# Kernel optimization log

Hardware: AMD Instinct MI355X
Metric: run time of the kernel (lower is better)

## Reference

```python
import jax, jax.numpy as jnp
import numpy as np

N = 8192        # number of routed items
D_IN = 1024     # sub-op output feature size (identity sub-ops)
E = 1024        # encoding_size
K = 8           # number of ops / type keys


def setup_inputs() -> dict:
    key = jax.random.key(0)
    k1, k2, k3, k4 = jax.random.split(key, 4)
    x = jax.random.normal(k1, (N, D_IN), dtype=jnp.float32)
    type_ids = jax.random.randint(k2, (N,), 0, K, dtype=jnp.int64)
    # Stacked per-type Linear params: Ws[k] maps op-k features -> encoding.
    W = jax.random.normal(k3, (K, D_IN, E), dtype=jnp.float32) / np.sqrt(D_IN)
    b = jax.random.normal(k4, (K, E), dtype=jnp.float32) * 0.01
    return {"x": x, "type_ids": type_ids, "W": W, "b": b}


def reference(x, type_ids, W, b):
    # x: [N, D], type_ids: [N] in [0, K), W: [K, D, E], b: [K, E]
    k = W.shape[0]
    onehot = jax.nn.one_hot(type_ids, k, dtype=x.dtype)          # [N, K] routing mask
    y = jnp.einsum('nd,kde->kne', x, W) + b[:, None, :]          # [K, N, E] per-type Linear
    enc = jnp.einsum('kne,nk->ne', y, onehot)                    # scatter-combine by type
    # out[:, :E] = routed encoding; out[:, E+ki] = 1.0 for item's type (one-hot tail)
    return jnp.concatenate([enc, onehot], axis=-1)               # [N, E + K]
```

## Files before the change

kernel.cpp:

```cpp
#include <hip/hip_runtime.h>

#define N_ITEMS 8192
#define D_IN    1024
#define E_OUT   1024
#define K_TYPES 8
#define OUT_W   (E_OUT + K_TYPES)

#define XBF_OFF  34816
#define WBF_OFF  (XBF_OFF + 16777216)
#define WS_NEED  ((size_t)WBF_OFF + 16777216)

typedef __attribute__((ext_vector_type(8))) short          bf16x8;
typedef __attribute__((ext_vector_type(8))) unsigned short u16x8;
typedef __attribute__((ext_vector_type(4))) float          f32x4;

__device__ __forceinline__ unsigned short f2bf(float f) {
    unsigned int u = __float_as_uint(f);
    return (unsigned short)((u + 0x7FFFu + ((u >> 16) & 1u)) >> 16);
}

__device__ __forceinline__ void gload16(const void* g, void* l) {
    __builtin_amdgcn_global_load_lds(
        (const __attribute__((address_space(1))) unsigned int*)g,
        (__attribute__((address_space(3)))       unsigned int*)l, 16, 0, 0);
}


__global__ __launch_bounds__(256) void k_sortmeta(const int* __restrict__ tid,
                                                  int* __restrict__ ws) {
    __shared__ int cnt[K_TYPES];
    const int t = threadIdx.x;
    if (t < K_TYPES) { cnt[t] = 0; ws[8 + t] = 0; }
    __syncthreads();
    int c[K_TYPES];
    #pragma unroll
    for (int k = 0; k < K_TYPES; ++k) c[k] = 0;
    for (int it = 0; it < N_ITEMS / 256; ++it) {
        const int v = tid[it * 256 + t];
        #pragma unroll
        for (int k = 0; k < K_TYPES; ++k) c[k] += (v == k) ? 1 : 0;
    }
    #pragma unroll
    for (int k = 0; k < K_TYPES; ++k) atomicAdd(&cnt[k], c[k]);
    __syncthreads();
    if (t == 0) {
        int off = 0, nt = 0;
        for (int k = 0; k < K_TYPES; ++k) {
            ws[16 + k] = off;
            const int cc = cnt[k];
            for (int r = 0; r < cc; r += 128) {
                ws[32 + 2 * nt] = k;
                ws[33 + 2 * nt] = off + r;
                ++nt;
            }
            off += cc;
        }
        ws[24] = off;
        ws[25] = nt;
    }
}

__global__ __launch_bounds__(256) void k_convX(const float* __restrict__ X,
                                               const int*   __restrict__ tid,
                                               int* __restrict__ ws,
                                               float* __restrict__ out) {
    __shared__ int wcnt[4][K_TYPES];
    __shared__ int wbase[4][K_TYPES];
    const int t = threadIdx.x;
    const int b = blockIdx.x;
    unsigned short* Xbf = (unsigned short*)((char*)ws + XBF_OFF);

    const size_t c0 = (size_t)b * 8192 + (size_t)t * 8;
    float4 v[8];
    #pragma unroll
    for (int j = 0; j < 4; ++j) {
        v[2 * j]     = *(const float4*)(X + c0 + (size_t)j * 2048);
        v[2 * j + 1] = *(const float4*)(X + c0 + (size_t)j * 2048 + 4);
    }
    #pragma unroll
    for (int j = 0; j < 4; ++j) {
        u16x8 o;
        o[0] = f2bf(v[2 * j].x);     o[1] = f2bf(v[2 * j].y);
        o[2] = f2bf(v[2 * j].z);     o[3] = f2bf(v[2 * j].w);
        o[4] = f2bf(v[2 * j + 1].x); o[5] = f2bf(v[2 * j + 1].y);
        o[6] = f2bf(v[2 * j + 1].z); o[7] = f2bf(v[2 * j + 1].w);
        *(u16x8*)(Xbf + c0 + (size_t)j * 2048) = o;
    }
    if (b < 32) {
        const int n    = b * 256 + t;
        const int v2   = tid[n];
        const int lane = t & 63;
        const int wv   = t >> 6;
        int myrank = 0;
        int mycnt  = 0;
        #pragma unroll
        for (int k = 0; k < K_TYPES; ++k) {
            const unsigned long long mk = __ballot(v2 == k);
            if (v2 == k)
                myrank = (int)__popcll(mk & ((1ull << lane) - 1ull));
            if (lane == k)
                mycnt = (int)__popcll(mk);
        }
        if (lane < K_TYPES) wcnt[wv][lane] = mycnt;
        __syncthreads();
        if (t < K_TYPES) {
            const int tot = wcnt[0][t] + wcnt[1][t] + wcnt[2][t] + wcnt[3][t];
            int base = ws[16 + t] + atomicAdd(&ws[8 + t], tot);
            #pragma unroll
            for (int q = 0; q < 4; ++q) { wbase[q][t] = base; base += wcnt[q][t]; }
        }
        __syncthreads();
        ws[256 + wbase[wv][v2] + myrank] = n;

        float* o2 = out + (size_t)n * OUT_W + E_OUT;
        *(float4*)(o2)     = make_float4(v2 == 0 ? 1.f : 0.f, v2 == 1 ? 1.f : 0.f,
                                         v2 == 2 ? 1.f : 0.f, v2 == 3 ? 1.f : 0.f);
        *(float4*)(o2 + 4) = make_float4(v2 == 4 ? 1.f : 0.f, v2 == 5 ? 1.f : 0.f,
                                         v2 == 6 ? 1.f : 0.f, v2 == 7 ? 1.f : 0.f);
    }
}

__global__ __launch_bounds__(256) void k_convW(const float* __restrict__ W,
                                               int* __restrict__ ws) {
    __shared__ unsigned short T[64][72];
    const int t = threadIdx.x;
    const int b = blockIdx.x;
    unsigned short* Wbf = (unsigned short*)((char*)ws + WBF_OFF);

    const int tbase = b * 2;
    const int dl = t >> 2;
    const int eq = (t & 3) * 16;
    float4 va[2][4];
    int kk[2], dd0[2], ee0[2];
    #pragma unroll
    for (int s = 0; s < 2; ++s) {
        const int tt = tbase + s;
        kk[s]  = tt >> 8;
        const int rem = tt & 255;
        dd0[s] = (rem >> 4) << 6;
        ee0[s] = (rem & 15) << 6;
        const float* src = W + ((size_t)(kk[s] * 1024 + dd0[s] + dl)) * 1024 + ee0[s] + eq;
        #pragma unroll
        for (int q = 0; q < 4; ++q)
            va[s][q] = *(const float4*)(src + q * 4);
    }
    const int el = t >> 2;
    const int dq = (t & 3) * 16;
    #pragma unroll
    for (int s = 0; s < 2; ++s) {
        if (s) __syncthreads();
        #pragma unroll
        for (int q = 0; q < 4; ++q) {
            T[eq + q * 4 + 0][dl] = f2bf(va[s][q].x);
            T[eq + q * 4 + 1][dl] = f2bf(va[s][q].y);
            T[eq + q * 4 + 2][dl] = f2bf(va[s][q].z);
            T[eq + q * 4 + 3][dl] = f2bf(va[s][q].w);
        }
        __syncthreads();
        unsigned short* dst = Wbf + ((size_t)kk[s] << 20)
                            + (size_t)(ee0[s] + el) * 1024 + dd0[s] + dq;
        *(u16x8*)(dst)     = *(const u16x8*)&T[el][dq];
        *(u16x8*)(dst + 8) = *(const u16x8*)&T[el][dq + 8];
    }
}

__global__ __launch_bounds__(256) void k_gemm_bf16(const float* __restrict__ Bias,
                                                   const int* __restrict__ ws,
                                                   float* __restrict__ out) {
    __shared__ unsigned short As[128 * 64];
    __shared__ unsigned short Bs[64 * 64];

    const int tile = blockIdx.x;
    if (tile >= ws[25]) return;
    const int ktype     = ws[32 + 2 * tile];
    const int row_start = ws[33 + 2 * tile];
    const int rows      = min(128, ws[17 + ktype] - row_start);
    const int* __restrict__ sorted = ws + 256 + row_start;
    const int bn0 = blockIdx.y * 64;

    const unsigned short* __restrict__ Xbf =
        (const unsigned short*)((const char*)ws + XBF_OFF);
    const unsigned short* __restrict__ Wbf =
        (const unsigned short*)((const char*)ws + WBF_OFF);

    const int t    = threadIdx.x;
    const int lane = t & 63;
    const int w    = t >> 6;
    const int wr   = w >> 1, wc = w & 1;

    const int srow = lane >> 3;
    const int skq  = (lane & 7) * 8;

    const unsigned short* gA[4];
    unsigned short* lA[4];
    #pragma unroll
    for (int i = 0; i < 4; ++i) {
        const int ar = w * 32 + i * 8 + srow;
        const int cr = sorted[ar < rows ? ar : rows - 1];
        gA[i] = Xbf + (size_t)cr * 1024 + skq;
        lA[i] = As + (w * 32 + i * 8) * 64;
    }
    const unsigned short* gB[2];
    unsigned short* lB[2];
    #pragma unroll
    for (int i = 0; i < 2; ++i) {
        const int er = bn0 + w * 16 + i * 8 + srow;
        gB[i] = Wbf + ((size_t)ktype << 20) + (size_t)er * 1024 + skq;
        lB[i] = Bs + (w * 16 + i * 8) * 64;
    }

    const int frow = lane & 15;
    const int fko  = (lane >> 4) * 8;
    const unsigned short* aB  = As + (wr * 64 + frow) * 64 + fko;
    const unsigned short* bBp = Bs + (wc * 32 + frow) * 64 + fko;

    f32x4 acc[4][2];
    #pragma unroll
    for (int m = 0; m < 4; ++m)
        #pragma unroll
        for (int n = 0; n < 2; ++n)
            acc[m][n] = (f32x4){0.f, 0.f, 0.f, 0.f};

    for (int k0 = 0; k0 < D_IN; k0 += 64) {
        #pragma unroll
        for (int i = 0; i < 4; ++i) gload16(gA[i] + k0, lA[i]);
        #pragma unroll
        for (int i = 0; i < 2; ++i) gload16(gB[i] + k0, lB[i]);
        __syncthreads();
        bf16x8 af[2][4], bf_[2][2];
        #pragma unroll
        for (int ks = 0; ks < 2; ++ks) {
            #pragma unroll
            for (int m = 0; m < 4; ++m)
                af[ks][m]  = *(const bf16x8*)(aB  + m * 16 * 64 + ks * 32);
            #pragma unroll
            for (int n = 0; n < 2; ++n)
                bf_[ks][n] = *(const bf16x8*)(bBp + n * 16 * 64 + ks * 32);
        }
        #pragma unroll
        for (int ks = 0; ks < 2; ++ks)
            #pragma unroll
            for (int m = 0; m < 4; ++m)
                #pragma unroll
                for (int n = 0; n < 2; ++n)
                    acc[m][n] = __builtin_amdgcn_mfma_f32_16x16x32_bf16(
                        af[ks][m], bf_[ks][n], acc[m][n], 0, 0, 0);
        __syncthreads();
    }

    const int col = lane & 15;
    const int rq  = (lane >> 4) * 4;
    float bv[2];
    #pragma unroll
    for (int n = 0; n < 2; ++n)
        bv[n] = Bias[ktype * E_OUT + bn0 + wc * 32 + n * 16 + col];
    #pragma unroll
    for (int m = 0; m < 4; ++m)
        #pragma unroll
        for (int j = 0; j < 4; ++j) {
            const int lr = wr * 64 + m * 16 + rq + j;
            if (lr < rows) {
                float* o = out + (size_t)sorted[lr] * OUT_W + bn0 + wc * 32 + col;
                o[0]  = acc[m][0][j] + bv[0];
                o[16] = acc[m][1][j] + bv[1];
            }
        }
}


__global__ void k_init(int* __restrict__ ws) {
    int t = threadIdx.x;
    if (t < K_TYPES) { ws[t] = 0; ws[8 + t] = 0; }
    if (t == 0) ws[25] = 0;
}
__global__ void k_hist(const int* __restrict__ tid, int* __restrict__ ws) {
    int n = blockIdx.x * 256 + threadIdx.x;
    if (n < N_ITEMS) atomicAdd(&ws[tid[n]], 1);
}
__global__ void k_scan(int* __restrict__ ws) {
    if (threadIdx.x != 0 || blockIdx.x != 0) return;
    int off = 0, nt = 0;
    for (int k = 0; k < K_TYPES; ++k) {
        ws[16 + k] = off;
        int c = ws[k];
        for (int r = 0; r < c; r += 128) { ws[32 + 2 * nt] = k; ws[33 + 2 * nt] = off + r; ++nt; }
        off += c;
    }
    ws[24] = off; ws[25] = nt;
}
__global__ void k_scatter(const int* __restrict__ tid, int* __restrict__ ws) {
    int n = blockIdx.x * 256 + threadIdx.x;
    if (n >= N_ITEMS) return;
    int v = tid[n];
    int pos = ws[16 + v] + atomicAdd(&ws[8 + v], 1);
    ws[256 + pos] = n;
}
__global__ void k_tail(const int* __restrict__ tid, float* __restrict__ out) {
    int i = blockIdx.x * 256 + threadIdx.x;
    if (i >= N_ITEMS * K_TYPES) return;
    int n = i >> 3, j = i & 7;
    out[(size_t)n * OUT_W + E_OUT + j] = (tid[n] == j) ? 1.0f : 0.0f;
}
__global__ __launch_bounds__(256) void k_gemm(const float* __restrict__ X,
                                              const float* __restrict__ Wt,
                                              const float* __restrict__ Bias,
                                              const int* __restrict__ ws,
                                              float* __restrict__ out) {
    const int tile = blockIdx.x;
    if (tile >= ws[25]) return;
    const int ktype = ws[32 + 2 * tile];
    const int row_start = ws[33 + 2 * tile];
    const int rows = min(128, ws[17 + ktype] - row_start);
    const int* __restrict__ sorted = ws + 256 + row_start;
    const int bn0 = blockIdx.y * 128;
    __shared__ float As2[16][132];
    __shared__ float Bs2[16][132];
    const int t = threadIdx.x, tx = t & 15, ty = t >> 4;
    const int arow0 = t >> 2, arow1 = arow0 + 64, akq = t & 3;
    const int ra = sorted[(arow0 < rows) ? arow0 : 0];
    const int rb = sorted[(arow1 < rows) ? arow1 : 0];
    const float* xa = X + (size_t)ra * D_IN + akq * 4;
    const float* xb = X + (size_t)rb * D_IN + akq * 4;
    const int bdr = t >> 5, bc = (t & 31) * 4;
    const float* wbase = Wt + ((size_t)ktype * D_IN) * E_OUT + bn0;
    const float* w0 = wbase + (size_t)bdr * E_OUT + bc;
    const float* w1 = wbase + (size_t)(bdr + 8) * E_OUT + bc;
    float acc[8][8];
    #pragma unroll
    for (int i = 0; i < 8; ++i)
        #pragma unroll
        for (int j = 0; j < 8; ++j) acc[i][j] = 0.f;
    for (int k0 = 0; k0 < D_IN; k0 += 16) {
        const float4 a0 = *(const float4*)(xa + k0);
        const float4 a1 = *(const float4*)(xb + k0);
        const float4 b0 = *(const float4*)(w0 + (size_t)k0 * E_OUT);
        const float4 b1 = *(const float4*)(w1 + (size_t)k0 * E_OUT);
        __syncthreads();
        As2[akq * 4 + 0][arow0] = a0.x; As2[akq * 4 + 1][arow0] = a0.y;
        As2[akq * 4 + 2][arow0] = a0.z; As2[akq * 4 + 3][arow0] = a0.w;
        As2[akq * 4 + 0][arow1] = a1.x; As2[akq * 4 + 1][arow1] = a1.y;
        As2[akq * 4 + 2][arow1] = a1.z; As2[akq * 4 + 3][arow1] = a1.w;
        *(float4*)&Bs2[bdr][bc] = b0; *(float4*)&Bs2[bdr + 8][bc] = b1;
        __syncthreads();
        #pragma unroll
        for (int kk = 0; kk < 16; ++kk) {
            const float4 av0 = *(const float4*)&As2[kk][ty * 4];
            const float4 av1 = *(const float4*)&As2[kk][64 + ty * 4];
            const float4 bv0 = *(const float4*)&Bs2[kk][tx * 4];
            const float4 bv1 = *(const float4*)&Bs2[kk][64 + tx * 4];
            const float a[8] = {av0.x, av0.y, av0.z, av0.w, av1.x, av1.y, av1.z, av1.w};
            const float bb[8] = {bv0.x, bv0.y, bv0.z, bv0.w, bv1.x, bv1.y, bv1.z, bv1.w};
            #pragma unroll
            for (int i = 0; i < 8; ++i)
                #pragma unroll
                for (int j = 0; j < 8; ++j) acc[i][j] = fmaf(a[i], bb[j], acc[i][j]);
        }
    }
    const float* bias = Bias + ktype * E_OUT + bn0;
    const float4 bi0 = *(const float4*)&bias[tx * 4];
    const float4 bi1 = *(const float4*)&bias[64 + tx * 4];
    const float bb[8] = {bi0.x, bi0.y, bi0.z, bi0.w, bi1.x, bi1.y, bi1.z, bi1.w};
    #pragma unroll
    for (int i = 0; i < 8; ++i) {
        const int lr = (i >> 2) * 64 + ty * 4 + (i & 3);
        if (lr < rows) {
            float* o = out + (size_t)sorted[lr] * OUT_W + bn0;
            *(float4*)&o[tx * 4] = make_float4(acc[i][0] + bb[0], acc[i][1] + bb[1],
                                               acc[i][2] + bb[2], acc[i][3] + bb[3]);
            *(float4*)&o[64 + tx * 4] = make_float4(acc[i][4] + bb[4], acc[i][5] + bb[5],
                                                    acc[i][6] + bb[6], acc[i][7] + bb[7]);
        }
    }
}

extern "C" void kernel_launch(void* const* d_in, const int* in_sizes, int n_in,
                              void* d_out, int out_size, void* d_ws, size_t ws_size,
                              hipStream_t stream) {
    const float* x   = (const float*)d_in[0];
    const int*   tid = (const int*)d_in[1];
    const float* W   = (const float*)d_in[2];
    const float* b   = (const float*)d_in[3];
    float* out = (float*)d_out;
    int*   ws  = (int*)d_ws;

    if (ws_size >= WS_NEED) {
        k_sortmeta<<<1, 256, 0, stream>>>(tid, ws);
        k_convX<<<1024, 256, 0, stream>>>(x, tid, ws, out);
        k_convW<<<1024, 256, 0, stream>>>(W, ws);
        dim3 grid(72, 16);
        k_gemm_bf16<<<grid, 256, 0, stream>>>(b, ws, out);
    } else {
        k_init<<<1, 64, 0, stream>>>(ws);
        k_hist<<<N_ITEMS / 256, 256, 0, stream>>>(tid, ws);
        k_scan<<<1, 1, 0, stream>>>(ws);
        k_scatter<<<N_ITEMS / 256, 256, 0, stream>>>(tid, ws);
        k_tail<<<(N_ITEMS * K_TYPES) / 256, 256, 0, stream>>>(tid, out);
        dim3 grid(72, 8);
        k_gemm<<<grid, 256, 0, stream>>>(x, W, b, ws, out);
    }
}
```

Before: 181.3 us.

## Merge sort-metadata and conversion kernels into one launch; stage GEMM epilogue via LDS

Replaces the three preprocessing kernels (sort metadata, X conversion, W transpose-conversion) with a single 2049-block kernel. The scatter blocks now compute their own per-type prefix offsets by rescanning all type ids, so they no longer depend on metadata from a previous launch. One extra block builds the tile list. The GEMM epilogue also stages accumulators through shared memory so each row is written back as float4 stores instead of strided scalar stores. This removes two launch gaps and the serialising single-block kernel, at the cost of redundant histogram work in 32 blocks and extra LDS round trips and barriers in the epilogue.

```diff
diff --git a/kernel.cpp b/kernel.cpp
--- a/kernel.cpp
+++ b/kernel.cpp
@@ -26,28 +26,150 @@
 }
 
 
-__global__ __launch_bounds__(256) void k_sortmeta(const int* __restrict__ tid,
-                                                  int* __restrict__ ws) {
-    __shared__ int cnt[K_TYPES];
+__global__ __launch_bounds__(256) void k_conv(const float* __restrict__ X,
+                                              const float* __restrict__ W,
+                                              const int*   __restrict__ tid,
+                                              int* __restrict__ ws,
+                                              float* __restrict__ out) {
+    __shared__ unsigned short T[64][72];
+    __shared__ int hist[K_TYPES], pref[K_TYPES];
+    __shared__ int wcnt[4][K_TYPES], wbase[4][K_TYPES];
     const int t = threadIdx.x;
-    if (t < K_TYPES) { cnt[t] = 0; ws[8 + t] = 0; }
+    const int b = blockIdx.x;
+    unsigned short* Xbf = (unsigned short*)((char*)ws + XBF_OFF);
+    unsigned short* Wbf = (unsigned short*)((char*)ws + WBF_OFF);
+
+    if (b < 1024) {
+        const size_t c0 = (size_t)b * 8192 + (size_t)t * 8;
+        float4 v[8];
+        #pragma unroll
+        for (int j = 0; j < 4; ++j) {
+            v[2 * j]     = *(const float4*)(X + c0 + (size_t)j * 2048);
+            v[2 * j + 1] = *(const float4*)(X + c0 + (size_t)j * 2048 + 4);
+        }
+        #pragma unroll
+        for (int j = 0; j < 4; ++j) {
+            u16x8 o;
+            o[0] = f2bf(v[2 * j].x);     o[1] = f2bf(v[2 * j].y);
+            o[2] = f2bf(v[2 * j].z);     o[3] = f2bf(v[2 * j].w);
+            o[4] = f2bf(v[2 * j + 1].x); o[5] = f2bf(v[2 * j + 1].y);
+            o[6] = f2bf(v[2 * j + 1].z); o[7] = f2bf(v[2 * j + 1].w);
+            *(u16x8*)(Xbf + c0 + (size_t)j * 2048) = o;
+        }
+        if (b < 32) {
+            if (t < K_TYPES) { hist[t] = 0; pref[t] = 0; }
+            __syncthreads();
+            int c[K_TYPES], p[K_TYPES];
+            #pragma unroll
+            for (int k = 0; k < K_TYPES; ++k) { c[k] = 0; p[k] = 0; }
+            const int mylo = b * 256;
+            for (int it = 0; it < N_ITEMS / 256; ++it) {
+                const int idx = it * 256 + t;
+                const int vv  = tid[idx];
+                const int before = (idx < mylo) ? 1 : 0;
+                #pragma unroll
+                for (int k = 0; k < K_TYPES; ++k) {
+                    const int is = (vv == k) ? 1 : 0;
+                    c[k] += is;
+                    p[k] += is & before;
+                }
+            }
+            #pragma unroll
+            for (int k = 0; k < K_TYPES; ++k) {
+                atomicAdd(&hist[k], c[k]);
+                atomicAdd(&pref[k], p[k]);
+            }
+            const int n    = mylo + t;
+            const int v2   = tid[n];
+            const int lane = t & 63;
+            const int wv   = t >> 6;
+            int myrank = 0, mycnt = 0;
+            #pragma unroll
+            for (int k = 0; k < K_TYPES; ++k) {
+                const unsigned long long mk = __ballot(v2 == k);
+                if (v2 == k)
+                    myrank = (int)__popcll(mk & ((1ull << lane) - 1ull));
+                if (lane == k)
+                    mycnt = (int)__popcll(mk);
+            }
+            if (lane < K_TYPES) wcnt[wv][lane] = mycnt;
+            __syncthreads();
+            if (t < K_TYPES) {
+                int off = 0;
+                for (int k2 = 0; k2 < t; ++k2) off += hist[k2];
+                int base = off + pref[t];
+                #pragma unroll
+                for (int q = 0; q < 4; ++q) { wbase[q][t] = base; base += wcnt[q][t]; }
+            }
+            __syncthreads();
+            ws[256 + wbase[wv][v2] + myrank] = n;
+
+            float* o2 = out + (size_t)n * OUT_W + E_OUT;
+            *(float4*)(o2)     = make_float4(v2 == 0 ? 1.f : 0.f, v2 == 1 ? 1.f : 0.f,
+                                             v2 == 2 ? 1.f : 0.f, v2 == 3 ? 1.f : 0.f);
+            *(float4*)(o2 + 4) = make_float4(v2 == 4 ? 1.f : 0.f, v2 == 5 ? 1.f : 0.f,
+                                             v2 == 6 ? 1.f : 0.f, v2 == 7 ? 1.f : 0.f);
+        }
+        return;
+    }
+
+    if (b < 2048) {
+        const int tbase = (b - 1024) * 2;
+        const int dl = t >> 2;
+        const int eq = (t & 3) * 16;
+        float4 va[2][4];
+        int kk[2], dd0[2], ee0[2];
+        #pragma unroll
+        for (int s = 0; s < 2; ++s) {
+            const int tt = tbase + s;
+            kk[s]  = tt >> 8;
+            const int rem = tt & 255;
+            dd0[s] = (rem >> 4) << 6;
+            ee0[s] = (rem & 15) << 6;
+            const float* src = W + ((size_t)(kk[s] * 1024 + dd0[s] + dl)) * 1024 + ee0[s] + eq;
+            #pragma unroll
+            for (int q = 0; q < 4; ++q)
+                va[s][q] = *(const float4*)(src + q * 4);
+        }
+        const int el = t >> 2;
+        const int dq = (t & 3) * 16;
+        #pragma unroll
+        for (int s = 0; s < 2; ++s) {
+            if (s) __syncthreads();
+            #pragma unroll
+            for (int q = 0; q < 4; ++q) {
+                T[eq + q * 4 + 0][dl] = f2bf(va[s][q].x);
+                T[eq + q * 4 + 1][dl] = f2bf(va[s][q].y);
+                T[eq + q * 4 + 2][dl] = f2bf(va[s][q].z);
+                T[eq + q * 4 + 3][dl] = f2bf(va[s][q].w);
+            }
+            __syncthreads();
+            unsigned short* dst = Wbf + ((size_t)kk[s] << 20)
+                                + (size_t)(ee0[s] + el) * 1024 + dd0[s] + dq;
+            *(u16x8*)(dst)     = *(const u16x8*)&T[el][dq];
+            *(u16x8*)(dst + 8) = *(const u16x8*)&T[el][dq + 8];
+        }
+        return;
+    }
+
+    if (t < K_TYPES) hist[t] = 0;
     __syncthreads();
     int c[K_TYPES];
     #pragma unroll
     for (int k = 0; k < K_TYPES; ++k) c[k] = 0;
     for (int it = 0; it < N_ITEMS / 256; ++it) {
-        const int v = tid[it * 256 + t];
-        #pragma unroll
-        for (int k = 0; k < K_TYPES; ++k) c[k] += (v == k) ? 1 : 0;
-    }
-    #pragma unroll
-    for (int k = 0; k < K_TYPES; ++k) atomicAdd(&cnt[k], c[k]);
+        const int vv = tid[it * 256 + t];
+        #pragma unroll
+        for (int k = 0; k < K_TYPES; ++k) c[k] += (vv == k) ? 1 : 0;
+    }
+    #pragma unroll
+    for (int k = 0; k < K_TYPES; ++k) atomicAdd(&hist[k], c[k]);
     __syncthreads();
     if (t == 0) {
         int off = 0, nt = 0;
         for (int k = 0; k < K_TYPES; ++k) {
             ws[16 + k] = off;
-            const int cc = cnt[k];
+            const int cc = hist[k];
             for (int r = 0; r < cc; r += 128) {
                 ws[32 + 2 * nt] = k;
                 ws[33 + 2 * nt] = off + r;
@@ -57,110 +179,6 @@
         }
         ws[24] = off;
         ws[25] = nt;
-    }
-}
-
-__global__ __launch_bounds__(256) void k_convX(const float* __restrict__ X,
-                                               const int*   __restrict__ tid,
-                                               int* __restrict__ ws,
-                                               float* __restrict__ out) {
-    __shared__ int wcnt[4][K_TYPES];
-    __shared__ int wbase[4][K_TYPES];
-    const int t = threadIdx.x;
-    const int b = blockIdx.x;
-    unsigned short* Xbf = (unsigned short*)((char*)ws + XBF_OFF);
-
-    const size_t c0 = (size_t)b * 8192 + (size_t)t * 8;
-    float4 v[8];
-    #pragma unroll
-    for (int j = 0; j < 4; ++j) {
-        v[2 * j]     = *(const float4*)(X + c0 + (size_t)j * 2048);
-        v[2 * j + 1] = *(const float4*)(X + c0 + (size_t)j * 2048 + 4);
-    }
-    #pragma unroll
-    for (int j = 0; j < 4; ++j) {
-        u16x8 o;
-        o[0] = f2bf(v[2 * j].x);     o[1] = f2bf(v[2 * j].y);
-        o[2] = f2bf(v[2 * j].z);     o[3] = f2bf(v[2 * j].w);
-        o[4] = f2bf(v[2 * j + 1].x); o[5] = f2bf(v[2 * j + 1].y);
-        o[6] = f2bf(v[2 * j + 1].z); o[7] = f2bf(v[2 * j + 1].w);
-        *(u16x8*)(Xbf + c0 + (size_t)j * 2048) = o;
-    }
-    if (b < 32) {
-        const int n    = b * 256 + t;
-        const int v2   = tid[n];
-        const int lane = t & 63;
-        const int wv   = t >> 6;
-        int myrank = 0;
-        int mycnt  = 0;
-        #pragma unroll
-        for (int k = 0; k < K_TYPES; ++k) {
-            const unsigned long long mk = __ballot(v2 == k);
-            if (v2 == k)
-                myrank = (int)__popcll(mk & ((1ull << lane) - 1ull));
-            if (lane == k)
-                mycnt = (int)__popcll(mk);
-        }
-        if (lane < K_TYPES) wcnt[wv][lane] = mycnt;
-        __syncthreads();
-        if (t < K_TYPES) {
-            const int tot = wcnt[0][t] + wcnt[1][t] + wcnt[2][t] + wcnt[3][t];
-            int base = ws[16 + t] + atomicAdd(&ws[8 + t], tot);
-            #pragma unroll
-            for (int q = 0; q < 4; ++q) { wbase[q][t] = base; base += wcnt[q][t]; }
-        }
-        __syncthreads();
-        ws[256 + wbase[wv][v2] + myrank] = n;
-
-        float* o2 = out + (size_t)n * OUT_W + E_OUT;
-        *(float4*)(o2)     = make_float4(v2 == 0 ? 1.f : 0.f, v2 == 1 ? 1.f : 0.f,
-                                         v2 == 2 ? 1.f : 0.f, v2 == 3 ? 1.f : 0.f);
-        *(float4*)(o2 + 4) = make_float4(v2 == 4 ? 1.f : 0.f, v2 == 5 ? 1.f : 0.f,
-                                         v2 == 6 ? 1.f : 0.f, v2 == 7 ? 1.f : 0.f);
-    }
-}
-
-__global__ __launch_bounds__(256) void k_convW(const float* __restrict__ W,
-                                               int* __restrict__ ws) {
-    __shared__ unsigned short T[64][72];
-    const int t = threadIdx.x;
-    const int b = blockIdx.x;
-    unsigned short* Wbf = (unsigned short*)((char*)ws + WBF_OFF);
-
-    const int tbase = b * 2;
-    const int dl = t >> 2;
-    const int eq = (t & 3) * 16;
-    float4 va[2][4];
-    int kk[2], dd0[2], ee0[2];
-    #pragma unroll
-    for (int s = 0; s < 2; ++s) {
-        const int tt = tbase + s;
-        kk[s]  = tt >> 8;
-        const int rem = tt & 255;
-        dd0[s] = (rem >> 4) << 6;
-        ee0[s] = (rem & 15) << 6;
-        const float* src = W + ((size_t)(kk[s] * 1024 + dd0[s] + dl)) * 1024 + ee0[s] + eq;
-        #pragma unroll
-        for (int q = 0; q < 4; ++q)
-            va[s][q] = *(const float4*)(src + q * 4);
-    }
-    const int el = t >> 2;
-    const int dq = (t & 3) * 16;
-    #pragma unroll
-    for (int s = 0; s < 2; ++s) {
-        if (s) __syncthreads();
-        #pragma unroll
-        for (int q = 0; q < 4; ++q) {
-            T[eq + q * 4 + 0][dl] = f2bf(va[s][q].x);
-            T[eq + q * 4 + 1][dl] = f2bf(va[s][q].y);
-            T[eq + q * 4 + 2][dl] = f2bf(va[s][q].z);
-            T[eq + q * 4 + 3][dl] = f2bf(va[s][q].w);
-        }
-        __syncthreads();
-        unsigned short* dst = Wbf + ((size_t)kk[s] << 20)
-                            + (size_t)(ee0[s] + el) * 1024 + dd0[s] + dq;
-        *(u16x8*)(dst)     = *(const u16x8*)&T[el][dq];
-        *(u16x8*)(dst + 8) = *(const u16x8*)&T[el][dq + 8];
     }
 }
 
@@ -250,21 +268,35 @@
 
     const int col = lane & 15;
     const int rq  = (lane >> 4) * 4;
-    float bv[2];
-    #pragma unroll
-    for (int n = 0; n < 2; ++n)
-        bv[n] = Bias[ktype * E_OUT + bn0 + wc * 32 + n * 16 + col];
-    #pragma unroll
-    for (int m = 0; m < 4; ++m)
-        #pragma unroll
-        for (int j = 0; j < 4; ++j) {
-            const int lr = wr * 64 + m * 16 + rq + j;
+    float* Cs = (float*)As;
+    const int rr = t >> 4;
+    const int c4 = (t & 15) * 4;
+    const float4 bv4 = *(const float4*)&Bias[ktype * E_OUT + bn0 + c4];
+    #pragma unroll
+    for (int ph = 0; ph < 2; ++ph) {
+        if (wr == ph) {
+            #pragma unroll
+            for (int m = 0; m < 4; ++m)
+                #pragma unroll
+                for (int n = 0; n < 2; ++n)
+                    #pragma unroll
+                    for (int j = 0; j < 4; ++j)
+                        Cs[(m * 16 + rq + j) * 64 + wc * 32 + n * 16 + col] =
+                            acc[m][n][j];
+        }
+        __syncthreads();
+        #pragma unroll
+        for (int rb = 0; rb < 4; ++rb) {
+            const int lr = ph * 64 + rb * 16 + rr;
             if (lr < rows) {
-                float* o = out + (size_t)sorted[lr] * OUT_W + bn0 + wc * 32 + col;
-                o[0]  = acc[m][0][j] + bv[0];
-                o[16] = acc[m][1][j] + bv[1];
-            }
-        }
+                const float4 vv = *(const float4*)&Cs[(rb * 16 + rr) * 64 + c4];
+                *(float4*)(out + (size_t)sorted[lr] * OUT_W + bn0 + c4) =
+                    make_float4(vv.x + bv4.x, vv.y + bv4.y,
+                                vv.z + bv4.z, vv.w + bv4.w);
+            }
+        }
+        __syncthreads();
+    }
 }
 
 
@@ -384,9 +416,7 @@
     int*   ws  = (int*)d_ws;
 
     if (ws_size >= WS_NEED) {
-        k_sortmeta<<<1, 256, 0, stream>>>(tid, ws);
-        k_convX<<<1024, 256, 0, stream>>>(x, tid, ws, out);
-        k_convW<<<1024, 256, 0, stream>>>(W, ws);
+        k_conv<<<2049, 256, 0, stream>>>(x, W, tid, ws, out);
         dim3 grid(72, 16);
         k_gemm_bf16<<<grid, 256, 0, stream>>>(b, ws, out);
     } else {
```

Result: no change. 183.1 us (+1.0%).
